# Performance work log

Hardware: AMD Instinct MI355X
Metric: run time of the kernel (lower is better)

Reference implementation:

```python
import jax, jax.numpy as jnp
import numpy as np

D_EMBED = 64
N_HEADS = 4
D_HEAD = D_EMBED // N_HEADS
D_FF = 96          # int(1.5 * d_embed)
D_MODEL = 128      # repeat_factor = d_model // d_embed = 2
EPS = 1e-5
B = 4
# (idx_start, kernel_size, channels_in, kernel_no) per layer of the source CNN
LAYERS = [(0, 9, 8, 256), (18688, 9, 16, 256), (55808, 9, 16, 512)]
N_PARAMS = 130048
MAX_SEQ = max(ks * cin for _, ks, cin, _ in LAYERS) + 1  # 145


def _kernel_indices(start, ks, cin, kno):
    # Static ragged slice indices: per kernel, its weights plus trailing bias.
    L = ks * cin
    base = start + np.arange(kno)[:, None] * L + np.arange(L)[None, :]
    bias = start + kno * L + np.arange(kno)
    return np.concatenate([base, bias[:, None]], axis=1)  # (kno, L+1)


_IDX = [jnp.asarray(_kernel_indices(*l)) for l in LAYERS]


def setup_inputs():
    key = jax.random.key(0)
    k = jax.random.split(key, 8)
    s = 1.0 / np.sqrt(D_EMBED)
    return {
        "x": jax.random.normal(k[0], (B, N_PARAMS), dtype=jnp.float32),
        "pos_emb": jax.random.normal(k[1], (MAX_SEQ, D_EMBED), dtype=jnp.float32) * s,
        "comp_token": jax.random.normal(k[2], (D_EMBED,), dtype=jnp.float32),
        "in_proj_w": jax.random.normal(k[3], (3 * D_EMBED, D_EMBED), dtype=jnp.float32) * s,
        "in_proj_b": jnp.zeros((3 * D_EMBED,), jnp.float32),
        "out_proj_w": jax.random.normal(k[4], (D_EMBED, D_EMBED), dtype=jnp.float32) * s,
        "out_proj_b": jnp.zeros((D_EMBED,), jnp.float32),
        "lin1_w": jax.random.normal(k[5], (D_FF, D_EMBED), dtype=jnp.float32) * s,
        "lin1_b": jnp.zeros((D_FF,), jnp.float32),
        "lin2_w": jax.random.normal(k[6], (D_EMBED, D_FF), dtype=jnp.float32) / np.sqrt(D_FF),
        "lin2_b": jnp.zeros((D_EMBED,), jnp.float32),
        "ln1_w": jnp.ones((D_EMBED,), jnp.float32),
        "ln1_b": jnp.zeros((D_EMBED,), jnp.float32),
        "ln2_w": jnp.ones((D_EMBED,), jnp.float32),
        "ln2_b": jnp.zeros((D_EMBED,), jnp.float32),
    }


def _layernorm(x, w, b):
    mu = jnp.mean(x, axis=-1, keepdims=True)
    var = jnp.mean(jnp.square(x - mu), axis=-1, keepdims=True)
    return (x - mu) * jax.lax.rsqrt(var + EPS) * w + b


def _encoder(t, in_proj_w, in_proj_b, out_proj_w, out_proj_b,
             lin1_w, lin1_b, lin2_w, lin2_b, ln1_w, ln1_b, ln2_w, ln2_b):
    # Post-norm TransformerEncoderLayer (relu, eval mode -> dropout = identity).
    M, S, _ = t.shape
    qkv = t @ in_proj_w.T + in_proj_b                     # (M, S, 3D)
    q, k, v = jnp.split(qkv, 3, axis=-1)
    heads = lambda u: u.reshape(M, S, N_HEADS, D_HEAD).transpose(0, 2, 1, 3)
    q, k, v = heads(q), heads(k), heads(v)
    attn = jax.nn.softmax(jnp.einsum('mhsd,mhtd->mhst', q, k) / np.sqrt(D_HEAD))
    o = jnp.einsum('mhst,mhtd->mhsd', attn, v).transpose(0, 2, 1, 3).reshape(M, S, D_EMBED)
    o = o @ out_proj_w.T + out_proj_b
    h = _layernorm(t + o, ln1_w, ln1_b)
    ff = jax.nn.relu(h @ lin1_w.T + lin1_b) @ lin2_w.T + lin2_b
    return _layernorm(h + ff, ln2_w, ln2_b)


def reference(x, pos_emb, comp_token, in_proj_w, in_proj_b, out_proj_w, out_proj_b,
              lin1_w, lin1_b, lin2_w, lin2_b, ln1_w, ln1_b, ln2_w, ln2_b):
    enc = (in_proj_w, in_proj_b, out_proj_w, out_proj_b,
           lin1_w, lin1_b, lin2_w, lin2_b, ln1_w, ln1_b, ln2_w, ln2_b)
    outs = []
    for idx in _IDX:  # fixed small loop over layers; kernels within a layer are batched
        K, n = idx.shape
        w = x[:, idx]                                     # (B, K, n) ragged gather
        tok = w[..., None] + pos_emb[:n]                  # scalar -> d_embed broadcast + pos add
        cls = jnp.broadcast_to(comp_token, (B, K, 1, D_EMBED))
        tok = jnp.concatenate([cls, tok], axis=2).reshape(B * K, n + 1, D_EMBED)
        y = _encoder(tok, *enc)[:, 0, :]                  # comp-token readout
        outs.append(y.reshape(B, K, D_EMBED))
    y = jnp.concatenate(outs, axis=1)                     # (B, 1024, d_embed)
    return jnp.tile(y, (1, 1, D_MODEL // D_EMBED))        # (B, 1024, d_model)
```

## Files before the change

kernel.cpp:

```cpp
#include <hip/hip_runtime.h>
#include <math.h>

#define NPAR 130048
#define EPSF 1e-5f

typedef _Float16 hfp;
typedef _Float16 h2x __attribute__((ext_vector_type(2)));
typedef _Float16 h4x __attribute__((ext_vector_type(4)));
typedef float    f4x __attribute__((ext_vector_type(4)));

#define BSTR  164
#define VSTR2 172
#define ATSTR 172
#define WOSTR 76
#define L2STRH 108

#define OFF_VPOST 0
#define OFF_WO    5504
#define OFF_L1    7936
#define OFF_L2    11584
#define OFF_BETA  15040
#define OFF_SM    15696
#define SM_CT   0
#define SM_BO   64
#define SM_B1   128
#define SM_B2   224
#define SM_LN1W 288
#define SM_LN1B 352
#define SM_LN2W 416
#define SM_LN2B 480
#define SM_ALPH 544
#define SM_GAM  548
#define STAGE_FLOATS 16400
#define OFF_W    16400
#define OFF_WB   18704
#define OFF_ATT  18720
#define OFF_INVS 24224
#define OFF_O    24288
#define OFF_H1   24896
#define OFF_R    25504
#define OFF_PRE  26368
#define OFF_RED  27456
#define LDS_FLOATS 27472

template<int C>
__device__ __forceinline__ float dppf(float x) {
    return __int_as_float(__builtin_amdgcn_update_dpp(0, __float_as_int(x), C, 0xf, 0xf, false));
}
__device__ __forceinline__ float rowsum16(float x) {
    x += dppf<0x128>(x); x += dppf<0x124>(x); x += dppf<0x122>(x); x += dppf<0x121>(x);
    return x;
}
__device__ __forceinline__ unsigned packh2(float a, float b) {
    union { h2x h; unsigned u; } cv;
    cv.h.x = (hfp)a; cv.h.y = (hfp)b;
    return cv.u;
}

__global__ __launch_bounds__(64) void k_pre(const float* __restrict__ pe,
                                            const float* __restrict__ ct,
                                            const float* __restrict__ W,
                                            const float* __restrict__ bq,
                                            const float* __restrict__ Wo,
                                            const float* __restrict__ bo,
                                            const float* __restrict__ L1w,
                                            const float* __restrict__ b1,
                                            const float* __restrict__ L2w,
                                            const float* __restrict__ b2,
                                            const float* __restrict__ ln1w,
                                            const float* __restrict__ ln1b,
                                            const float* __restrict__ ln2w,
                                            const float* __restrict__ ln2b,
                                            float* __restrict__ ws)
{
    const int j = blockIdx.x;
    const int o = threadIdx.x;
    hfp* wsh = (hfp*)ws;

    if (j < 145) {
        const float4* wq4 = (const float4*)(W + o*64);
        const float4* wk4 = (const float4*)(W + (64 + o)*64);
        const float4* wv4 = (const float4*)(W + (128 + o)*64);
        const float4* p4  = (const float4*)(pe + j*64);
        float sk = bq[64 + o], sv = bq[128 + o], sq = bq[o];
        #pragma unroll
        for (int e = 0; e < 16; ++e) {
            float4 k4 = wk4[e], v4 = wv4[e], q4 = wq4[e], pp = p4[e];
            float4 cc = ((const float4*)ct)[e];
            sk += k4.x*pp.x + k4.y*pp.y + k4.z*pp.z + k4.w*pp.w;
            sv += v4.x*pp.x + v4.y*pp.y + v4.z*pp.z + v4.w*pp.w;
            sq += q4.x*cc.x + q4.y*cc.y + q4.z*cc.z + q4.w*cc.w;
        }
        wsh[o*VSTR2 + j] = (hfp)sv;
        float r = sq * sk;
        #pragma unroll
        for (int off = 1; off < 16; off <<= 1) r += __shfl_xor(r, off);
        if ((o & 15) == 0) ws[OFF_BETA + (o >> 4)*BSTR + j] = r;
    } else if (j == 145) {
        const float4* wq4 = (const float4*)(W + o*64);
        const float4* wk4 = (const float4*)(W + (64 + o)*64);
        const float4* wv4 = (const float4*)(W + (128 + o)*64);
        float sq = bq[o], sk = bq[64 + o], sv = bq[128 + o], suk = 0.f, suv = 0.f;
        #pragma unroll
        for (int e = 0; e < 16; ++e) {
            float4 k4 = wk4[e], v4 = wv4[e], q4 = wq4[e];
            float4 cc = ((const float4*)ct)[e];
            sq += q4.x*cc.x + q4.y*cc.y + q4.z*cc.z + q4.w*cc.w;
            sk += k4.x*cc.x + k4.y*cc.y + k4.z*cc.z + k4.w*cc.w;
            sv += v4.x*cc.x + v4.y*cc.y + v4.z*cc.z + v4.w*cc.w;
            suk += k4.x + k4.y + k4.z + k4.w;
            suv += v4.x + v4.y + v4.z + v4.w;
        }
        wsh[o*VSTR2 + 156] = (hfp)sv;
        wsh[o*VSTR2 + 157] = (hfp)suv;
        #pragma unroll
        for (int c = 145; c < 156; ++c) wsh[o*VSTR2 + c] = (hfp)0.f;
        wsh[o*VSTR2 + 158] = (hfp)0.f;
        wsh[o*VSTR2 + 159] = (hfp)0.f;
        float a = sq * suk, g = sq * sk;
        #pragma unroll
        for (int off = 1; off < 16; off <<= 1) {
            a += __shfl_xor(a, off);
            g += __shfl_xor(g, off);
        }
        if ((o & 15) == 0) {
            ws[OFF_SM + SM_ALPH + (o >> 4)] = a;
            ws[OFF_SM + SM_GAM  + (o >> 4)] = g;
        }
    } else if (j == 146) {
        ws[OFF_SM + SM_CT   + o] = ct[o];
        ws[OFF_SM + SM_BO   + o] = bo[o];
        ws[OFF_SM + SM_B2   + o] = b2[o];
        ws[OFF_SM + SM_LN1W + o] = ln1w[o];
        ws[OFF_SM + SM_LN1B + o] = ln1b[o];
        ws[OFF_SM + SM_LN2W + o] = ln2w[o];
        ws[OFF_SM + SM_LN2B + o] = ln2b[o];
        ws[OFF_SM + SM_B1   + o] = b1[o];
        if (o < 32) ws[OFF_SM + SM_B1 + 64 + o] = b1[64 + o];
    } else if (j == 147) {
        for (int idx = o; idx < 4096; idx += 64)
            wsh[OFF_WO*2 + (idx >> 6)*WOSTR + (idx & 63)] = (hfp)Wo[idx];
    } else if (j == 148) {
        for (int idx = o; idx < 6144; idx += 64)
            wsh[OFF_L1*2 + (idx >> 6)*WOSTR + (idx & 63)] = (hfp)L1w[idx];
    } else {
        for (int idx = o; idx < 6144; idx += 64) {
            int r = idx / 96, c = idx - r*96;
            wsh[OFF_L2*2 + r*L2STRH + c] = (hfp)L2w[idx];
        }
    }
}

template<int L>
__device__ __forceinline__ void run_group(const float* __restrict__ x,
                                          float* __restrict__ lds,
                                          float* __restrict__ out,
                                          int b, int k0, int start, int kno, int kgo)
{
    const int tid  = threadIdx.x;
    const int wave = tid >> 6;
    const int lane = tid & 63;
    const int e16  = lane & 15;
    const int g4   = (lane >> 4) * 4;
    const hfp* ldsh = (const hfp*)lds;
    const float* sm = lds + OFF_SM;

    {
        const f4x* src = (const f4x*)(x + (size_t)b*NPAR + start + (size_t)k0*L);
        f4x* dst = (f4x*)(lds + OFF_W);
        #pragma unroll
        for (int c = 0; c < (4*L + 255)/256; ++c) {
            int i4 = c*256 + tid;
            if (i4 < 4*L) dst[i4] = src[i4];
        }
        if (tid < 16) lds[OFF_WB + tid] = x[(size_t)b*NPAR + start + (size_t)kno*L + k0 + tid];
    }
    __syncthreads();

    {
        float wm = 0.f;
        for (int i = tid; i < 16*L; i += 256) wm = fmaxf(wm, fabsf(lds[OFF_W + i]));
        if (tid < 16) wm = fmaxf(wm, fabsf(lds[OFF_WB + tid]));
        #pragma unroll
        for (int off = 1; off < 64; off <<= 1) wm = fmaxf(wm, __shfl_xor(wm, off));
        if (lane == 0) lds[OFF_RED + wave] = wm;
        float mb = -1e30f;
        for (int j = lane; j < 145; j += 64) mb = fmaxf(mb, lds[OFF_BETA + wave*BSTR + j]);
        #pragma unroll
        for (int off = 1; off < 64; off <<= 1) mb = fmaxf(mb, __shfl_xor(mb, off));
        if (lane == 0) lds[OFF_RED + 8 + wave] = mb;
    }
    __syncthreads();

    {
        const float wmax = fmaxf(fmaxf(lds[OFF_RED+0], lds[OFF_RED+1]),
                                 fmaxf(lds[OFF_RED+2], lds[OFF_RED+3]));
        const int r = tid >> 2;
        const int m = r >> 2, h = r & 3, q = tid & 3;
        const float alpha = sm[SM_ALPH + h];
        const float gam   = sm[SM_GAM  + h];
        const float mbh   = lds[OFF_RED + 8 + h];
        const float M = fmaxf(0.25f*(fabsf(alpha)*wmax + mbh), 0.25f*gam);
        unsigned* arow32 = (unsigned*)(lds + OFF_ATT) + r*(ATSTR/2);
        const float* wr = lds + OFF_W + m*L;
        const float* br = lds + OFF_BETA + h*BSTR;
        float S = 0.f, WS = 0.f;
        #pragma unroll
        for (int t = 0; t < 10; ++t) {
            const int j0 = 16*t + 4*q;
            if (16*t + 15 < L || j0 + 3 < L) {
                f4x wv = *(const f4x*)(wr + j0);
                f4x bv = *(const f4x*)(br + j0);
                float p0 = __expf(fmaf(alpha, wv.x, bv.x)*0.25f - M);
                float p1 = __expf(fmaf(alpha, wv.y, bv.y)*0.25f - M);
                float p2 = __expf(fmaf(alpha, wv.z, bv.z)*0.25f - M);
                float p3 = __expf(fmaf(alpha, wv.w, bv.w)*0.25f - M);
                S  += (p0 + p1) + (p2 + p3);
                WS += (p0*wv.x + p1*wv.y) + (p2*wv.z + p3*wv.w);
                uint2 u; u.x = packh2(p0, p1); u.y = packh2(p2, p3);
                *(uint2*)(arow32 + (j0 >> 1)) = u;
            } else if (j0 <= L) {
                float pv4[4] = {0.f, 0.f, 0.f, 0.f};
                #pragma unroll
                for (int ee = 0; ee < 4; ++ee) {
                    int j = j0 + ee;
                    if (j <= L) {
                        float w = (j < L) ? wr[j] : lds[OFF_WB + m];
                        float p = __expf(fmaf(alpha, w, br[j])*0.25f - M);
                        S += p; WS += p*w; pv4[ee] = p;
                    }
                }
                uint2 u; u.x = packh2(pv4[0], pv4[1]); u.y = packh2(pv4[2], pv4[3]);
                *(uint2*)(arow32 + (j0 >> 1)) = u;
            } else if (j0 != 156) {
                uint2 z; z.x = 0u; z.y = 0u;
                *(uint2*)(arow32 + (j0 >> 1)) = z;
            }
        }
        S  += __shfl_xor(S, 1);  S  += __shfl_xor(S, 2);
        WS += __shfl_xor(WS, 1); WS += __shfl_xor(WS, 2);
        const float pc = __expf(0.25f*gam - M);
        S += pc;
        if (q == 0) {
            lds[OFF_INVS + r] = 1.f / S;
            arow32[78] = packh2(pc, WS);
            arow32[79] = 0u;
        }
    }
    __syncthreads();

    {
        const hfp* atth = ldsh + OFF_ATT*2;
        const int hh = wave;
        f4x vacc = (f4x){0.f,0.f,0.f,0.f};
        #pragma unroll
        for (int kt = 0; kt < 10; ++kt) {
            h4x a  = *(const h4x*)(atth + (e16*4 + hh)*ATSTR + kt*16 + g4);
            h4x bf = *(const h4x*)(ldsh + (16*hh + e16)*VSTR2 + kt*16 + g4);
            vacc = __builtin_amdgcn_mfma_f32_16x16x16f16(a, bf, vacc, 0, 0, 0);
        }
        hfp* Oh = (hfp*)(lds + OFF_O);
        #pragma unroll
        for (int rr = 0; rr < 4; ++rr) {
            float sc = lds[OFF_INVS + (g4 + rr)*4 + hh];
            Oh[(g4 + rr)*WOSTR + 16*hh + e16] = (hfp)(vacc[rr] * sc);
        }
    }
    __syncthreads();

    {
        const hfp* Oh  = ldsh + OFF_O*2;
        const hfp* Woh = ldsh + OFF_WO*2;
        const int tn = wave;
        f4x pacc = (f4x){0.f,0.f,0.f,0.f};
        #pragma unroll
        for (int kt = 0; kt < 4; ++kt) {
            h4x a  = *(const h4x*)(Oh + e16*WOSTR + kt*16 + g4);
            h4x bf = *(const h4x*)(Woh + (16*tn + e16)*WOSTR + kt*16 + g4);
            pacc = __builtin_amdgcn_mfma_f32_16x16x16f16(a, bf, pacc, 0, 0, 0);
        }
        const int n = 16*tn + e16;
        const float add = sm[SM_BO + n] + sm[SM_CT + n];
        #pragma unroll
        for (int rr = 0; rr < 4; ++rr)
            lds[OFF_PRE + (g4 + rr)*68 + n] = pacc[rr] + add;
    }
    __syncthreads();

    {
        const int m  = wave*4 + (lane >> 4);
        const int c0 = (lane & 15) * 4;
        f4x pv = *(const f4x*)(lds + OFF_PRE + m*68 + c0);
        float s = (pv.x + pv.y) + (pv.z + pv.w);
        float mu = rowsum16(s) * (1.f/64.f);
        f4x d; d.x = pv.x-mu; d.y = pv.y-mu; d.z = pv.z-mu; d.w = pv.w-mu;
        float v = (d.x*d.x + d.y*d.y) + (d.z*d.z + d.w*d.w);
        float rs = rsqrtf(rowsum16(v)*(1.f/64.f) + EPSF);
        f4x lw = *(const f4x*)(sm + SM_LN1W + c0);
        f4x lb = *(const f4x*)(sm + SM_LN1B + c0);
        h4x hv;
        hv.x = (hfp)(d.x*rs*lw.x + lb.x);
        hv.y = (hfp)(d.y*rs*lw.y + lb.y);
        hv.z = (hfp)(d.z*rs*lw.z + lb.z);
        hv.w = (hfp)(d.w*rs*lw.w + lb.w);
        *(h4x*)((hfp*)(lds + OFF_H1) + m*WOSTR + c0) = hv;
    }
    __syncthreads();

    {
        const hfp* H1h = ldsh + OFF_H1*2;
        const hfp* L1h = ldsh + OFF_L1*2;
        h4x af[4];
        #pragma unroll
        for (int kt = 0; kt < 4; ++kt) af[kt] = *(const h4x*)(H1h + e16*WOSTR + kt*16 + g4);
        hfp* Rh = (hfp*)(lds + OFF_R);
        #pragma unroll
        for (int u = 0; u < 2; ++u) {
            const int tt = wave + u*4;
            if (tt < 6) {
                f4x racc = (f4x){0.f,0.f,0.f,0.f};
                #pragma unroll
                for (int kt = 0; kt < 4; ++kt) {
                    h4x bf = *(const h4x*)(L1h + (16*tt + e16)*WOSTR + kt*16 + g4);
                    racc = __builtin_amdgcn_mfma_f32_16x16x16f16(af[kt], bf, racc, 0, 0, 0);
                }
                const int n = 16*tt + e16;
                const float bb = sm[SM_B1 + n];
                #pragma unroll
                for (int rr = 0; rr < 4; ++rr)
                    Rh[(g4 + rr)*L2STRH + n] = (hfp)fmaxf(racc[rr] + bb, 0.f);
            }
        }
    }
    __syncthreads();

    {
        const hfp* Rh2 = ldsh + OFF_R*2;
        const hfp* L2h = ldsh + OFF_L2*2;
        const int tn = wave;
        h4x af[6];
        #pragma unroll
        for (int kt = 0; kt < 6; ++kt) af[kt] = *(const h4x*)(Rh2 + e16*L2STRH + kt*16 + g4);
        f4x yacc = (f4x){0.f,0.f,0.f,0.f};
        #pragma unroll
        for (int kt = 0; kt < 6; ++kt) {
            h4x bf = *(const h4x*)(L2h + (16*tn + e16)*L2STRH + kt*16 + g4);
            yacc = __builtin_amdgcn_mfma_f32_16x16x16f16(af[kt], bf, yacc, 0, 0, 0);
        }
        const int n = 16*tn + e16;
        const float bb = sm[SM_B2 + n];
        #pragma unroll
        for (int rr = 0; rr < 4; ++rr)
            lds[OFF_PRE + (g4 + rr)*68 + n] = yacc[rr] + bb;
    }
    __syncthreads();

    {
        const int m  = wave*4 + (lane >> 4);
        const int c0 = (lane & 15) * 4;
        f4x pv = *(const f4x*)(lds + OFF_PRE + m*68 + c0);
        h4x h1p = *(const h4x*)((const hfp*)(lds + OFF_H1) + m*WOSTR + c0);
        f4x tot;
        tot.x = pv.x + (float)h1p.x;
        tot.y = pv.y + (float)h1p.y;
        tot.z = pv.z + (float)h1p.z;
        tot.w = pv.w + (float)h1p.w;
        float s = (tot.x + tot.y) + (tot.z + tot.w);
        float mu = rowsum16(s) * (1.f/64.f);
        f4x d; d.x = tot.x-mu; d.y = tot.y-mu; d.z = tot.z-mu; d.w = tot.w-mu;
        float v = (d.x*d.x + d.y*d.y) + (d.z*d.z + d.w*d.w);
        float rs = rsqrtf(rowsum16(v)*(1.f/64.f) + EPSF);
        f4x lw = *(const f4x*)(sm + SM_LN2W + c0);
        f4x lb = *(const f4x*)(sm + SM_LN2B + c0);
        f4x y;
        y.x = d.x*rs*lw.x + lb.x;
        y.y = d.y*rs*lw.y + lb.y;
        y.z = d.z*rs*lw.z + lb.z;
        y.w = d.w*rs*lw.w + lb.w;
        float* ob = out + ((size_t)b*1024 + kgo + k0 + m)*128;
        *(f4x*)(ob + c0)      = y;
        *(f4x*)(ob + 64 + c0) = y;
    }
}

__global__ __launch_bounds__(256, 1) void k_main(const float* __restrict__ x,
                                                 const float* __restrict__ ws,
                                                 float* __restrict__ out)
{
    __shared__ __align__(16) float lds[LDS_FLOATS];
    const int tid = threadIdx.x;

    {
        const f4x* src = (const f4x*)ws;
        f4x* dst = (f4x*)lds;
        #pragma unroll
        for (int c = 0; c < 17; ++c) {
            int i4 = c*256 + tid;
            if (i4 < STAGE_FLOATS/4) dst[i4] = src[i4];
        }
    }

    const int w = blockIdx.x;
    if (w < 64) {
        run_group<72>(x, lds, out, w >> 4, (w & 15)*16, 0, 256, 0);
    } else if (w < 128) {
        const int w2 = w - 64;
        run_group<144>(x, lds, out, w2 >> 4, (w2 & 15)*16, 18688, 256, 256);
    } else {
        const int w3 = w - 128;
        run_group<144>(x, lds, out, w3 >> 5, (w3 & 31)*16, 55808, 512, 512);
    }
}

extern "C" void kernel_launch(void* const* d_in, const int* in_sizes, int n_in,
                              void* d_out, int out_size, void* d_ws, size_t ws_size,
                              hipStream_t stream) {
    const float* x    = (const float*)d_in[0];
    const float* pe   = (const float*)d_in[1];
    const float* ct   = (const float*)d_in[2];
    const float* Wq   = (const float*)d_in[3];
    const float* bq   = (const float*)d_in[4];
    const float* Wo   = (const float*)d_in[5];
    const float* bo   = (const float*)d_in[6];
    const float* L1w  = (const float*)d_in[7];
    const float* b1   = (const float*)d_in[8];
    const float* L2w  = (const float*)d_in[9];
    const float* b2   = (const float*)d_in[10];
    const float* ln1w = (const float*)d_in[11];
    const float* ln1b = (const float*)d_in[12];
    const float* ln2w = (const float*)d_in[13];
    const float* ln2b = (const float*)d_in[14];
    float* out = (float*)d_out;
    float* ws  = (float*)d_ws;

    k_pre <<<150, 64, 0, stream>>>(pe, ct, Wq, bq, Wo, bo, L1w, b1, L2w, b2,
                                   ln1w, ln1b, ln2w, ln2b, ws);
    k_main<<<256, 256, 0, stream>>>(x, ws, out);
}
```

Measured before the change: 19.84 us.

## Load MFMA weight fragments straight into registers instead of staging to LDS

Each block no longer copies the ~64KB precomputed workspace into LDS. MFMA B-operand fragments for V, Wo, L1 and L2 and the small bias and LayerNorm vectors are instead read from global memory (likely L2-resident) into registers up front, and beta is read directly from global. The abs-max reduction over the input weights is fused into the global-to-LDS load, which drops one barrier, and the bo+ct sum is precomputed. This shrinks LDS footprint and removes the staging copy, at the cost of higher register pressure and global-latency reads of beta inside the softmax loop.

```diff
diff --git a/kernel.cpp b/kernel.cpp
--- a/kernel.cpp
+++ b/kernel.cpp
@@ -31,17 +31,18 @@
 #define SM_LN2B 480
 #define SM_ALPH 544
 #define SM_GAM  548
-#define STAGE_FLOATS 16400
-#define OFF_W    16400
-#define OFF_WB   18704
-#define OFF_ATT  18720
-#define OFF_INVS 24224
-#define OFF_O    24288
-#define OFF_H1   24896
-#define OFF_R    25504
-#define OFF_PRE  26368
-#define OFF_RED  27456
-#define LDS_FLOATS 27472
+#define SM_BOCT 576
+
+#define L_W    0
+#define L_WB   2304
+#define L_ATT  2320
+#define L_INVS 7824
+#define L_O    7888
+#define L_H1   8496
+#define L_R    9104
+#define L_PRE  9968
+#define L_RED  11056
+#define LDS_FLOATS 11072
 
 template<int C>
 __device__ __forceinline__ float dppf(float x) {
@@ -130,6 +131,7 @@
     } else if (j == 146) {
         ws[OFF_SM + SM_CT   + o] = ct[o];
         ws[OFF_SM + SM_BO   + o] = bo[o];
+        ws[OFF_SM + SM_BOCT + o] = bo[o] + ct[o];
         ws[OFF_SM + SM_B2   + o] = b2[o];
         ws[OFF_SM + SM_LN1W + o] = ln1w[o];
         ws[OFF_SM + SM_LN1B + o] = ln1b[o];
@@ -153,6 +155,7 @@
 
 template<int L>
 __device__ __forceinline__ void run_group(const float* __restrict__ x,
+                                          const float* __restrict__ ws,
                                           float* __restrict__ lds,
                                           float* __restrict__ out,
                                           int b, int k0, int start, int kno, int kgo)
@@ -162,48 +165,87 @@
     const int lane = tid & 63;
     const int e16  = lane & 15;
     const int g4   = (lane >> 4) * 4;
+    const int c0   = e16 * 4;
+    const hfp* wsh  = (const hfp*)ws;
     const hfp* ldsh = (const hfp*)lds;
-    const float* sm = lds + OFF_SM;
-
+
+    float wm = 0.f;
     {
         const f4x* src = (const f4x*)(x + (size_t)b*NPAR + start + (size_t)k0*L);
-        f4x* dst = (f4x*)(lds + OFF_W);
+        f4x* dst = (f4x*)(lds + L_W);
         #pragma unroll
         for (int c = 0; c < (4*L + 255)/256; ++c) {
             int i4 = c*256 + tid;
-            if (i4 < 4*L) dst[i4] = src[i4];
-        }
-        if (tid < 16) lds[OFF_WB + tid] = x[(size_t)b*NPAR + start + (size_t)kno*L + k0 + tid];
-    }
-    __syncthreads();
-
-    {
-        float wm = 0.f;
-        for (int i = tid; i < 16*L; i += 256) wm = fmaxf(wm, fabsf(lds[OFF_W + i]));
-        if (tid < 16) wm = fmaxf(wm, fabsf(lds[OFF_WB + tid]));
+            if (i4 < 4*L) {
+                f4x v = src[i4];
+                dst[i4] = v;
+                wm = fmaxf(wm, fmaxf(fmaxf(fabsf(v.x), fabsf(v.y)), fmaxf(fabsf(v.z), fabsf(v.w))));
+            }
+        }
+        if (tid < 16) {
+            float bwv = x[(size_t)b*NPAR + start + (size_t)kno*L + k0 + tid];
+            lds[L_WB + tid] = bwv;
+            wm = fmaxf(wm, fabsf(bwv));
+        }
+    }
+
+    h4x vpf[10];
+    #pragma unroll
+    for (int kt = 0; kt < 10; ++kt)
+        vpf[kt] = *(const h4x*)(wsh + (16*wave + e16)*VSTR2 + kt*16 + g4);
+    h4x wof[4];
+    #pragma unroll
+    for (int kt = 0; kt < 4; ++kt)
+        wof[kt] = *(const h4x*)(wsh + OFF_WO*2 + (16*wave + e16)*WOSTR + kt*16 + g4);
+    h4x l1f[2][4];
+    float b1v[2];
+    #pragma unroll
+    for (int u = 0; u < 2; ++u) {
+        const int tt = wave + 4*u;
+        if (tt < 6) {
+            #pragma unroll
+            for (int kt = 0; kt < 4; ++kt)
+                l1f[u][kt] = *(const h4x*)(wsh + OFF_L1*2 + (16*tt + e16)*WOSTR + kt*16 + g4);
+            b1v[u] = ws[OFF_SM + SM_B1 + 16*tt + e16];
+        }
+    }
+    h4x l2f[6];
+    #pragma unroll
+    for (int kt = 0; kt < 6; ++kt)
+        l2f[kt] = *(const h4x*)(wsh + OFF_L2*2 + (16*wave + e16)*L2STRH + kt*16 + g4);
+    const int nw = 16*wave + e16;
+    const float boct = ws[OFF_SM + SM_BOCT + nw];
+    const float b2v  = ws[OFF_SM + SM_B2   + nw];
+    const int hsm = (tid >> 2) & 3;
+    const float alpha = ws[OFF_SM + SM_ALPH + hsm];
+    const float gam   = ws[OFF_SM + SM_GAM  + hsm];
+    const f4x ln1w4 = *(const f4x*)(ws + OFF_SM + SM_LN1W + c0);
+    const f4x ln1b4 = *(const f4x*)(ws + OFF_SM + SM_LN1B + c0);
+    const f4x ln2w4 = *(const f4x*)(ws + OFF_SM + SM_LN2W + c0);
+    const f4x ln2b4 = *(const f4x*)(ws + OFF_SM + SM_LN2B + c0);
+
+    {
         #pragma unroll
         for (int off = 1; off < 64; off <<= 1) wm = fmaxf(wm, __shfl_xor(wm, off));
-        if (lane == 0) lds[OFF_RED + wave] = wm;
+        if (lane == 0) lds[L_RED + wave] = wm;
         float mb = -1e30f;
-        for (int j = lane; j < 145; j += 64) mb = fmaxf(mb, lds[OFF_BETA + wave*BSTR + j]);
+        for (int j = lane; j < 145; j += 64) mb = fmaxf(mb, ws[OFF_BETA + wave*BSTR + j]);
         #pragma unroll
         for (int off = 1; off < 64; off <<= 1) mb = fmaxf(mb, __shfl_xor(mb, off));
-        if (lane == 0) lds[OFF_RED + 8 + wave] = mb;
-    }
-    __syncthreads();
-
-    {
-        const float wmax = fmaxf(fmaxf(lds[OFF_RED+0], lds[OFF_RED+1]),
-                                 fmaxf(lds[OFF_RED+2], lds[OFF_RED+3]));
+        if (lane == 0) lds[L_RED + 8 + wave] = mb;
+    }
+    __syncthreads();
+
+    {
+        const float wmax = fmaxf(fmaxf(lds[L_RED+0], lds[L_RED+1]),
+                                 fmaxf(lds[L_RED+2], lds[L_RED+3]));
         const int r = tid >> 2;
         const int m = r >> 2, h = r & 3, q = tid & 3;
-        const float alpha = sm[SM_ALPH + h];
-        const float gam   = sm[SM_GAM  + h];
-        const float mbh   = lds[OFF_RED + 8 + h];
+        const float mbh = lds[L_RED + 8 + h];
         const float M = fmaxf(0.25f*(fabsf(alpha)*wmax + mbh), 0.25f*gam);
-        unsigned* arow32 = (unsigned*)(lds + OFF_ATT) + r*(ATSTR/2);
-        const float* wr = lds + OFF_W + m*L;
-        const float* br = lds + OFF_BETA + h*BSTR;
+        unsigned* arow32 = (unsigned*)(lds + L_ATT) + r*(ATSTR/2);
+        const float* wr = lds + L_W + m*L;
+        const float* br = ws + OFF_BETA + h*BSTR;
         float S = 0.f, WS = 0.f;
         #pragma unroll
         for (int t = 0; t < 10; ++t) {
@@ -225,7 +267,7 @@
                 for (int ee = 0; ee < 4; ++ee) {
                     int j = j0 + ee;
                     if (j <= L) {
-                        float w = (j < L) ? wr[j] : lds[OFF_WB + m];
+                        float w = (j < L) ? wr[j] : lds[L_WB + m];
                         float p = __expf(fmaf(alpha, w, br[j])*0.25f - M);
                         S += p; WS += p*w; pv4[ee] = p;
                     }
@@ -242,7 +284,7 @@
         const float pc = __expf(0.25f*gam - M);
         S += pc;
         if (q == 0) {
-            lds[OFF_INVS + r] = 1.f / S;
+            lds[L_INVS + r] = 1.f / S;
             arow32[78] = packh2(pc, WS);
             arow32[79] = 0u;
         }
@@ -250,116 +292,95 @@
     __syncthreads();
 
     {
-        const hfp* atth = ldsh + OFF_ATT*2;
+        const hfp* atth = ldsh + L_ATT*2;
         const int hh = wave;
         f4x vacc = (f4x){0.f,0.f,0.f,0.f};
         #pragma unroll
         for (int kt = 0; kt < 10; ++kt) {
-            h4x a  = *(const h4x*)(atth + (e16*4 + hh)*ATSTR + kt*16 + g4);
-            h4x bf = *(const h4x*)(ldsh + (16*hh + e16)*VSTR2 + kt*16 + g4);
-            vacc = __builtin_amdgcn_mfma_f32_16x16x16f16(a, bf, vacc, 0, 0, 0);
-        }
-        hfp* Oh = (hfp*)(lds + OFF_O);
+            h4x a = *(const h4x*)(atth + (e16*4 + hh)*ATSTR + kt*16 + g4);
+            vacc = __builtin_amdgcn_mfma_f32_16x16x16f16(a, vpf[kt], vacc, 0, 0, 0);
+        }
+        hfp* Oh = (hfp*)(lds + L_O);
         #pragma unroll
         for (int rr = 0; rr < 4; ++rr) {
-            float sc = lds[OFF_INVS + (g4 + rr)*4 + hh];
+            float sc = lds[L_INVS + (g4 + rr)*4 + hh];
             Oh[(g4 + rr)*WOSTR + 16*hh + e16] = (hfp)(vacc[rr] * sc);
         }
     }
     __syncthreads();
 
     {
-        const hfp* Oh  = ldsh + OFF_O*2;
-        const hfp* Woh = ldsh + OFF_WO*2;
-        const int tn = wave;
+        const hfp* Oh = ldsh + L_O*2;
         f4x pacc = (f4x){0.f,0.f,0.f,0.f};
         #pragma unroll
         for (int kt = 0; kt < 4; ++kt) {
-            h4x a  = *(const h4x*)(Oh + e16*WOSTR + kt*16 + g4);
-            h4x bf = *(const h4x*)(Woh + (16*tn + e16)*WOSTR + kt*16 + g4);
-            pacc = __builtin_amdgcn_mfma_f32_16x16x16f16(a, bf, pacc, 0, 0, 0);
-        }
-        const int n = 16*tn + e16;
-        const float add = sm[SM_BO + n] + sm[SM_CT + n];
+            h4x a = *(const h4x*)(Oh + e16*WOSTR + kt*16 + g4);
+            pacc = __builtin_amdgcn_mfma_f32_16x16x16f16(a, wof[kt], pacc, 0, 0, 0);
+        }
         #pragma unroll
         for (int rr = 0; rr < 4; ++rr)
-            lds[OFF_PRE + (g4 + rr)*68 + n] = pacc[rr] + add;
-    }
-    __syncthreads();
-
-    {
-        const int m  = wave*4 + (lane >> 4);
-        const int c0 = (lane & 15) * 4;
-        f4x pv = *(const f4x*)(lds + OFF_PRE + m*68 + c0);
+            lds[L_PRE + (g4 + rr)*68 + nw] = pacc[rr] + boct;
+    }
+    __syncthreads();
+
+    {
+        const int m = wave*4 + (lane >> 4);
+        f4x pv = *(const f4x*)(lds + L_PRE + m*68 + c0);
         float s = (pv.x + pv.y) + (pv.z + pv.w);
         float mu = rowsum16(s) * (1.f/64.f);
         f4x d; d.x = pv.x-mu; d.y = pv.y-mu; d.z = pv.z-mu; d.w = pv.w-mu;
         float v = (d.x*d.x + d.y*d.y) + (d.z*d.z + d.w*d.w);
         float rs = rsqrtf(rowsum16(v)*(1.f/64.f) + EPSF);
-        f4x lw = *(const f4x*)(sm + SM_LN1W + c0);
-        f4x lb = *(const f4x*)(sm + SM_LN1B + c0);
         h4x hv;
-        hv.x = (hfp)(d.x*rs*lw.x + lb.x);
-        hv.y = (hfp)(d.y*rs*lw.y + lb.y);
-        hv.z = (hfp)(d.z*rs*lw.z + lb.z);
-        hv.w = (hfp)(d.w*rs*lw.w + lb.w);
-        *(h4x*)((hfp*)(lds + OFF_H1) + m*WOSTR + c0) = hv;
-    }
-    __syncthreads();
-
-    {
-        const hfp* H1h = ldsh + OFF_H1*2;
-        const hfp* L1h = ldsh + OFF_L1*2;
+        hv.x = (hfp)(d.x*rs*ln1w4.x + ln1b4.x);
+        hv.y = (hfp)(d.y*rs*ln1w4.y + ln1b4.y);
+        hv.z = (hfp)(d.z*rs*ln1w4.z + ln1b4.z);
+        hv.w = (hfp)(d.w*rs*ln1w4.w + ln1b4.w);
+        *(h4x*)((hfp*)(lds + L_H1) + m*WOSTR + c0) = hv;
+    }
+    __syncthreads();
+
+    {
+        const hfp* H1h = ldsh + L_H1*2;
         h4x af[4];
         #pragma unroll
         for (int kt = 0; kt < 4; ++kt) af[kt] = *(const h4x*)(H1h + e16*WOSTR + kt*16 + g4);
-        hfp* Rh = (hfp*)(lds + OFF_R);
+        hfp* Rh = (hfp*)(lds + L_R);
         #pragma unroll
         for (int u = 0; u < 2; ++u) {
-            const int tt = wave + u*4;
+            const int tt = wave + 4*u;
             if (tt < 6) {
                 f4x racc = (f4x){0.f,0.f,0.f,0.f};
                 #pragma unroll
-                for (int kt = 0; kt < 4; ++kt) {
-                    h4x bf = *(const h4x*)(L1h + (16*tt + e16)*WOSTR + kt*16 + g4);
-                    racc = __builtin_amdgcn_mfma_f32_16x16x16f16(af[kt], bf, racc, 0, 0, 0);
-                }
+                for (int kt = 0; kt < 4; ++kt)
+                    racc = __builtin_amdgcn_mfma_f32_16x16x16f16(af[kt], l1f[u][kt], racc, 0, 0, 0);
                 const int n = 16*tt + e16;
-                const float bb = sm[SM_B1 + n];
                 #pragma unroll
                 for (int rr = 0; rr < 4; ++rr)
-                    Rh[(g4 + rr)*L2STRH + n] = (hfp)fmaxf(racc[rr] + bb, 0.f);
+                    Rh[(g4 + rr)*L2STRH + n] = (hfp)fmaxf(racc[rr] + b1v[u], 0.f);
             }
         }
     }
     __syncthreads();
 
     {
-        const hfp* Rh2 = ldsh + OFF_R*2;
-        const hfp* L2h = ldsh + OFF_L2*2;
-        const int tn = wave;
-        h4x af[6];
-        #pragma unroll
-        for (int kt = 0; kt < 6; ++kt) af[kt] = *(const h4x*)(Rh2 + e16*L2STRH + kt*16 + g4);
+        const hfp* Rh2 = ldsh + L_R*2;
         f4x yacc = (f4x){0.f,0.f,0.f,0.f};
         #pragma unroll
         for (int kt = 0; kt < 6; ++kt) {
-            h4x bf = *(const h4x*)(L2h + (16*tn + e16)*L2STRH + kt*16 + g4);
-            yacc = __builtin_amdgcn_mfma_f32_16x16x16f16(af[kt], bf, yacc, 0, 0, 0);
-        }
-        const int n = 16*tn + e16;
-        const float bb = sm[SM_B2 + n];
+            h4x a = *(const h4x*)(Rh2 + e16*L2STRH + kt*16 + g4);
+            yacc = __builtin_amdgcn_mfma_f32_16x16x16f16(a, l2f[kt], yacc, 0, 0, 0);
+        }
         #pragma unroll
         for (int rr = 0; rr < 4; ++rr)
-            lds[OFF_PRE + (g4 + rr)*68 + n] = yacc[rr] + bb;
-    }
-    __syncthreads();
-
-    {
-        const int m  = wave*4 + (lane >> 4);
-        const int c0 = (lane & 15) * 4;
-        f4x pv = *(const f4x*)(lds + OFF_PRE + m*68 + c0);
-        h4x h1p = *(const h4x*)((const hfp*)(lds + OFF_H1) + m*WOSTR + c0);
+            lds[L_PRE + (g4 + rr)*68 + nw] = yacc[rr] + b2v;
+    }
+    __syncthreads();
+
+    {
+        const int m = wave*4 + (lane >> 4);
+        f4x pv = *(const f4x*)(lds + L_PRE + m*68 + c0);
+        h4x h1p = *(const h4x*)((const hfp*)(lds + L_H1) + m*WOSTR + c0);
         f4x tot;
         tot.x = pv.x + (float)h1p.x;
         tot.y = pv.y + (float)h1p.y;
@@ -370,13 +391,11 @@
         f4x d; d.x = tot.x-mu; d.y = tot.y-mu; d.z = tot.z-mu; d.w = tot.w-mu;
         float v = (d.x*d.x + d.y*d.y) + (d.z*d.z + d.w*d.w);
         float rs = rsqrtf(rowsum16(v)*(1.f/64.f) + EPSF);
-        f4x lw = *(const f4x*)(sm + SM_LN2W + c0);
-        f4x lb = *(const f4x*)(sm + SM_LN2B + c0);
         f4x y;
-        y.x = d.x*rs*lw.x + lb.x;
-        y.y = d.y*rs*lw.y + lb.y;
-        y.z = d.z*rs*lw.z + lb.z;
-        y.w = d.w*rs*lw.w + lb.w;
+        y.x = d.x*rs*ln2w4.x + ln2b4.x;
+        y.y = d.y*rs*ln2w4.y + ln2b4.y;
+        y.z = d.z*rs*ln2w4.z + ln2b4.z;
+        y.w = d.w*rs*ln2w4.w + ln2b4.w;
         float* ob = out + ((size_t)b*1024 + kgo + k0 + m)*128;
         *(f4x*)(ob + c0)      = y;
         *(f4x*)(ob + 64 + c0) = y;
@@ -388,27 +407,15 @@
                                                  float* __restrict__ out)
 {
     __shared__ __align__(16) float lds[LDS_FLOATS];
-    const int tid = threadIdx.x;
-
-    {
-        const f4x* src = (const f4x*)ws;
-        f4x* dst = (f4x*)lds;
-        #pragma unroll
-        for (int c = 0; c < 17; ++c) {
-            int i4 = c*256 + tid;
-            if (i4 < STAGE_FLOATS/4) dst[i4] = src[i4];
-        }
-    }
-
     const int w = blockIdx.x;
     if (w < 64) {
-        run_group<72>(x, lds, out, w >> 4, (w & 15)*16, 0, 256, 0);
+        run_group<72>(x, ws, lds, out, w >> 4, (w & 15)*16, 0, 256, 0);
     } else if (w < 128) {
         const int w2 = w - 64;
-        run_group<144>(x, lds, out, w2 >> 4, (w2 & 15)*16, 18688, 256, 256);
+        run_group<144>(x, ws, lds, out, w2 >> 4, (w2 & 15)*16, 18688, 256, 256);
     } else {
         const int w3 = w - 128;
-        run_group<144>(x, lds, out, w3 >> 5, (w3 & 31)*16, 55808, 512, 512);
+        run_group<144>(x, ws, lds, out, w3 >> 5, (w3 & 31)*16, 55808, 512, 512);
     }
 }
 
```

New measurement: 19.40 us. 1.02x faster.
